# Kernel optimization log

Measured on AMD Instinct MI355X. Metric: run time of the kernel, lower is better.

## Reference

```python
import jax, jax.numpy as jnp
import numpy as np

X_DIM, Y_DIM, HIDDEN, N = 768, 768, 300, 768


def setup_inputs() -> dict:
    key = jax.random.key(0)
    ks = jax.random.split(key, 7)
    lim1 = 1.0 / np.sqrt(X_DIM + Y_DIM)
    lim2 = 1.0 / np.sqrt(HIDDEN)
    return {
        "x_samples": jax.random.normal(ks[0], (N, X_DIM), dtype=jnp.float32),
        "y_samples": jax.random.normal(ks[1], (N, Y_DIM), dtype=jnp.float32),
        "perm": jax.random.permutation(ks[2], N).astype(jnp.int32),
        # Linear 1: (x_dim+y_dim) -> hidden, torch default uniform init
        "W1": jax.random.uniform(ks[3], (HIDDEN, X_DIM + Y_DIM), jnp.float32, -lim1, lim1),
        "b1": jax.random.uniform(ks[4], (HIDDEN,), jnp.float32, -lim1, lim1),
        # Linear 2: hidden -> 1
        "W2": jax.random.uniform(ks[5], (1, HIDDEN), jnp.float32, -lim2, lim2),
        "b2": jax.random.uniform(ks[6], (1,), jnp.float32, -lim2, lim2),
    }


def reference(x_samples, y_samples, perm, W1, b1, W2, b2):
    n = x_samples.shape[0]
    x_dim = x_samples.shape[1]
    # First linear is separable across the concat: split W1 into x- and y-parts.
    hx = x_samples @ W1[:, :x_dim].T            # [N, H]
    hy = y_samples @ W1[:, x_dim:].T            # [N, H]
    w2 = W2[0]                                   # [H]
    # T0: matched pairs (x_i, y_i)
    t0 = jax.nn.softplus(jax.nn.relu(hx + hy + b1) @ w2 + b2[0])   # [N]
    # T1[i, j] = F(x_j, y_perm[i]) -- pairwise tile, [N, N, H] intermediate
    hyp = hy[perm]                               # [N, H]
    hpair = jax.nn.relu(hyp[:, None, :] + hx[None, :, :] + b1)     # [N, N, H]
    t1 = jax.nn.softplus(hpair @ w2 + b2[0])     # [N, N]
    lower_bound = t0.mean() - (jax.nn.logsumexp(t1, axis=1).mean() - jnp.log(n).astype(t1.dtype))
    return lower_bound
```

## Files before the change

kernel.cpp:

```cpp
#include <hip/hip_runtime.h>
#include <math.h>

#define NN   768
#define HH   300
#define HP   320
#define KD   768

#define P_OFF    0
#define PKS_STR  245760
#define PG_STR   983040
#define CF_OFF   1966080
#define AF_OFF   2211840
#define RS_OFF   2457600
#define T0_OFF   2469888

__global__ __launch_bounds__(256) void k1_gemm(
    const float* __restrict__ x, const float* __restrict__ y,
    const int* __restrict__ perm, const float* __restrict__ W1,
    float* __restrict__ wsf)
{
    const int tid = threadIdx.x;
    const int tx = tid & 15;
    const int ty = tid >> 4;
    const int i0 = blockIdx.x * 128;
    const int h0 = blockIdx.y * 64;
    const int g  = blockIdx.z & 1;
    const int ks = blockIdx.z >> 1;
    const int kbeg = ks * 192;

    const float* src = g ? y : x;
    const int koff = g ? KD : 0;

    __shared__ float Xt[32][132];
    __shared__ float Wt[32][68];

    float acc[4][8];
    #pragma unroll
    for (int r = 0; r < 4; ++r)
        #pragma unroll
        for (int cc = 0; cc < 8; ++cc) acc[r][cc] = 0.f;

    const int kq = (tid & 7) << 2;
    const float* xp[4];
    int xr[4];
    #pragma unroll
    for (int it = 0; it < 4; ++it) {
        int row = ((tid + it*256) >> 3);
        int gr = i0 + row;
        if (g) gr = perm[gr];
        xp[it] = src + (size_t)gr * KD + kbeg + kq;
        xr[it] = row;
    }
    const float* wp[2];
    int wr[2]; bool wv[2];
    #pragma unroll
    for (int it = 0; it < 2; ++it) {
        int hrow = ((tid + it*256) >> 3);
        int hg = h0 + hrow;
        wv[it] = hg < HH;
        wp[it] = W1 + (size_t)(wv[it] ? hg : 0) * (2*KD) + koff + kbeg + kq;
        wr[it] = hrow;
    }

    for (int kb = 0; kb < 192; kb += 32) {
        float4 xv[4], wvv[2];
        #pragma unroll
        for (int it = 0; it < 4; ++it) xv[it] = *(const float4*)(xp[it] + kb);
        #pragma unroll
        for (int it = 0; it < 2; ++it) {
            wvv[it] = *(const float4*)(wp[it] + kb);
            if (!wv[it]) wvv[it] = make_float4(0,0,0,0);
        }
        if (kb) __syncthreads();
        #pragma unroll
        for (int it = 0; it < 4; ++it) {
            Xt[kq+0][xr[it]] = xv[it].x; Xt[kq+1][xr[it]] = xv[it].y;
            Xt[kq+2][xr[it]] = xv[it].z; Xt[kq+3][xr[it]] = xv[it].w;
        }
        #pragma unroll
        for (int it = 0; it < 2; ++it) {
            Wt[kq+0][wr[it]] = wvv[it].x; Wt[kq+1][wr[it]] = wvv[it].y;
            Wt[kq+2][wr[it]] = wvv[it].z; Wt[kq+3][wr[it]] = wvv[it].w;
        }
        __syncthreads();

        #pragma unroll 8
        for (int k = 0; k < 32; ++k) {
            float4 a   = *(const float4*)&Wt[k][4*ty];
            float4 b0  = *(const float4*)&Xt[k][4*tx];
            float4 b1v = *(const float4*)&Xt[k][64 + 4*tx];
            float ar[4] = {a.x, a.y, a.z, a.w};
            float br[8] = {b0.x, b0.y, b0.z, b0.w, b1v.x, b1v.y, b1v.z, b1v.w};
            #pragma unroll
            for (int r = 0; r < 4; ++r)
                #pragma unroll
                for (int cc = 0; cc < 8; ++cc)
                    acc[r][cc] = fmaf(ar[r], br[cc], acc[r][cc]);
        }
    }

    float* dst = wsf + P_OFF + (size_t)(g*4 + ks) * PKS_STR;
    #pragma unroll
    for (int cc = 0; cc < 8; ++cc) {
        int i = i0 + ((cc >> 2) ? 64 : 0) + 4*tx + (cc & 3);
        float4 v = make_float4(acc[0][cc], acc[1][cc], acc[2][cc], acc[3][cc]);
        *(float4*)(dst + (size_t)i * HP + h0 + 4*ty) = v;
    }
}

__global__ __launch_bounds__(256) void k1b_combine(
    const float* __restrict__ b1, float* __restrict__ wsf)
{
    int idx = blockIdx.x * 256 + threadIdx.x;
    int g = idx >= 61440;
    int rem = idx - g * 61440;
    int i = rem / 80;
    int h4 = (rem % 80) * 4;

    float4 o = make_float4(0.f,0.f,0.f,0.f);
    const float* p = wsf + P_OFF + (size_t)g * PG_STR + (size_t)i * HP + h4;
    #pragma unroll
    for (int ks = 0; ks < 4; ++ks) {
        float4 v = *(const float4*)(p + (size_t)ks * PKS_STR);
        o.x += v.x; o.y += v.y; o.z += v.z; o.w += v.w;
    }
    if (g && h4 < HH) {
        float4 bv = *(const float4*)(b1 + h4);
        o.x += bv.x; o.y += bv.y; o.z += bv.z; o.w += bv.w;
    }
    float* dst = wsf + (g ? AF_OFF : CF_OFF) + (size_t)i * HP + h4;
    *(float4*)dst = o;
}

__global__ __launch_bounds__(512, 2) void k2_pair(
    const float* __restrict__ wsf, const float* __restrict__ w2,
    const int* __restrict__ perm, const float* __restrict__ b2,
    float* __restrict__ rsO, float* __restrict__ t0c)
{
    const int tid  = threadIdx.x;
    const int half = tid >> 8;
    const int t2   = tid & 255;
    const int tx = t2 & 15;
    const int ty = t2 >> 4;
    const int j0 = blockIdx.x * 48;
    const int i0 = blockIdx.y * 48;
    const int hbeg = half * 152;

    const float* AF = wsf + AF_OFF;
    const float* CF = wsf + CF_OFF;

    __shared__ __align__(16) float As[2][48][156];
    __shared__ __align__(16) float Cs[2][48][156];
    __shared__ __align__(16) float w2s[304];

    if (tid < 76) {
        float4 wv = make_float4(0.f,0.f,0.f,0.f);
        if (tid < 75) wv = *(const float4*)(w2 + 4*tid);
        *(float4*)&w2s[4*tid] = wv;
    }
    for (int e = t2; e < 48 * 38; e += 256) {
        int i = e / 38, q = e % 38;
        *(float4*)&As[half][i][4*q] =
            *(const float4*)(AF + (size_t)(i0 + i) * HP + hbeg + 4*q);
        *(float4*)&Cs[half][i][4*q] =
            *(const float4*)(CF + (size_t)(j0 + i) * HP + hbeg + 4*q);
    }
    __syncthreads();

    float acc[3][3];
    #pragma unroll
    for (int r = 0; r < 3; ++r)
        #pragma unroll
        for (int c = 0; c < 3; ++c) acc[r][c] = 0.f;

    #pragma unroll 2
    for (int k = 0; k < 38; ++k) {
        float4 wq = *(const float4*)&w2s[hbeg + 4*k];
        float4 a0 = *(const float4*)&As[half][ty     ][4*k];
        float4 a1 = *(const float4*)&As[half][ty + 16][4*k];
        float4 a2 = *(const float4*)&As[half][ty + 32][4*k];
        float4 c0 = *(const float4*)&Cs[half][tx     ][4*k];
        float4 c1 = *(const float4*)&Cs[half][tx + 16][4*k];
        float4 c2 = *(const float4*)&Cs[half][tx + 32][4*k];
        const float* wp  = (const float*)&wq;
        const float* ap0 = (const float*)&a0;
        const float* ap1 = (const float*)&a1;
        const float* ap2 = (const float*)&a2;
        const float* cp0 = (const float*)&c0;
        const float* cp1 = (const float*)&c1;
        const float* cp2 = (const float*)&c2;
        #pragma unroll
        for (int hh = 0; hh < 4; ++hh) {
            float wh = wp[hh];
            float av0 = ap0[hh], av1 = ap1[hh], av2 = ap2[hh];
            float cv0 = cp0[hh], cv1 = cp1[hh], cv2 = cp2[hh];
            acc[0][0] = fmaf(fmaxf(av0 + cv0, 0.f), wh, acc[0][0]);
            acc[0][1] = fmaf(fmaxf(av0 + cv1, 0.f), wh, acc[0][1]);
            acc[0][2] = fmaf(fmaxf(av0 + cv2, 0.f), wh, acc[0][2]);
            acc[1][0] = fmaf(fmaxf(av1 + cv0, 0.f), wh, acc[1][0]);
            acc[1][1] = fmaf(fmaxf(av1 + cv1, 0.f), wh, acc[1][1]);
            acc[1][2] = fmaf(fmaxf(av1 + cv2, 0.f), wh, acc[1][2]);
            acc[2][0] = fmaf(fmaxf(av2 + cv0, 0.f), wh, acc[2][0]);
            acc[2][1] = fmaf(fmaxf(av2 + cv1, 0.f), wh, acc[2][1]);
            acc[2][2] = fmaf(fmaxf(av2 + cv2, 0.f), wh, acc[2][2]);
        }
    }

    __syncthreads();
    float* comb = &As[0][0][0];
    if (half) {
        float* cp = comb + t2 * 9;
        #pragma unroll
        for (int r = 0; r < 3; ++r)
            #pragma unroll
            for (int c = 0; c < 3; ++c) cp[r*3 + c] = acc[r][c];
    }
    __syncthreads();

    if (half == 0) {
        const float* cp = comb + t2 * 9;
        const float b2v = b2[0];
        #pragma unroll
        for (int r = 0; r < 3; ++r) {
            int i = i0 + ty + 16 * r;
            int pj = perm[i];
            float rsum = 0.f;
            #pragma unroll
            for (int c = 0; c < 3; ++c) {
                int j = j0 + tx + 16 * c;
                float u = acc[r][c] + cp[r*3 + c] + b2v;
                rsum += expf(u);
                if (j == pj)
                    t0c[i] = (u > 0.f) ? u + log1pf(expf(-u)) : log1pf(expf(u));
            }
            #pragma unroll
            for (int off = 8; off; off >>= 1)
                rsum += __shfl_xor(rsum, off, 16);
            if (tx == 0) rsO[(size_t)blockIdx.x * NN + i] = rsum;
        }
    }
}

__global__ __launch_bounds__(256) void k3_final(
    const float* __restrict__ wsf, float* __restrict__ out)
{
    const int tid = threadIdx.x;
    const float* rs = wsf + RS_OFF;
    const float* t0 = wsf + T0_OFF;

    double st0 = 0.0, slse = 0.0;
    for (int i = tid; i < NN; i += 256) {
        float s = 0.f;
        #pragma unroll
        for (int jb = 0; jb < 16; ++jb) s += rs[(size_t)jb * NN + i];
        st0  += (double)t0[i];
        slse += log((double)NN + (double)s);
    }
    __shared__ double sa[256], sb[256];
    sa[tid] = st0; sb[tid] = slse;
    __syncthreads();
    for (int s = 128; s > 0; s >>= 1) {
        if (tid < s) { sa[tid] += sa[tid+s]; sb[tid] += sb[tid+s]; }
        __syncthreads();
    }
    if (tid == 0) {
        double lb = sa[0]/(double)NN - (sb[0]/(double)NN - log((double)NN));
        out[0] = (float)lb;
    }
}

extern "C" void kernel_launch(void* const* d_in, const int* in_sizes, int n_in,
                              void* d_out, int out_size, void* d_ws, size_t ws_size,
                              hipStream_t stream) {
    const float* x    = (const float*)d_in[0];
    const float* y    = (const float*)d_in[1];
    const int*   perm = (const int*)  d_in[2];
    const float* W1   = (const float*)d_in[3];
    const float* b1   = (const float*)d_in[4];
    const float* W2   = (const float*)d_in[5];
    const float* b2   = (const float*)d_in[6];
    float* wsf = (float*)d_ws;
    float* out = (float*)d_out;

    k1_gemm    <<<dim3(6,5,8),  256, 0, stream>>>(x, y, perm, W1, wsf);
    k1b_combine<<<480,          256, 0, stream>>>(b1, wsf);
    k2_pair    <<<dim3(16,16),  512, 0, stream>>>(wsf, W2, perm, b2,
                                                  wsf + RS_OFF, wsf + T0_OFF);
    k3_final   <<<1,            256, 0, stream>>>(wsf, out);
}
```

Measured before the change: 115.5 us.

## Transpose pair-kernel LDS tiles to k-major and software-pipeline the inner loop

```diff
diff --git a/kernel.cpp b/kernel.cpp
--- a/kernel.cpp
+++ b/kernel.cpp
@@ -132,7 +132,33 @@
     *(float4*)dst = o;
 }
 
-__global__ __launch_bounds__(512, 2) void k2_pair(
+#define ROW(wv, a0v, a1v, a2v, c0v, c1v, c2v)                      \
+    acc00 = fmaf(fmaxf(a0v + c0v, 0.f), wv, acc00);                \
+    acc01 = fmaf(fmaxf(a0v + c1v, 0.f), wv, acc01);                \
+    acc02 = fmaf(fmaxf(a0v + c2v, 0.f), wv, acc02);                \
+    acc10 = fmaf(fmaxf(a1v + c0v, 0.f), wv, acc10);                \
+    acc11 = fmaf(fmaxf(a1v + c1v, 0.f), wv, acc11);                \
+    acc12 = fmaf(fmaxf(a1v + c2v, 0.f), wv, acc12);                \
+    acc20 = fmaf(fmaxf(a2v + c0v, 0.f), wv, acc20);                \
+    acc21 = fmaf(fmaxf(a2v + c1v, 0.f), wv, acc21);                \
+    acc22 = fmaf(fmaxf(a2v + c2v, 0.f), wv, acc22);
+
+#define COMPQ(W, A0, A1, A2, C0, C1, C2)                           \
+    ROW(W.x, A0.x, A1.x, A2.x, C0.x, C1.x, C2.x)                   \
+    ROW(W.y, A0.y, A1.y, A2.y, C0.y, C1.y, C2.y)                   \
+    ROW(W.z, A0.z, A1.z, A2.z, C0.z, C1.z, C2.z)                   \
+    ROW(W.w, A0.w, A1.w, A2.w, C0.w, C1.w, C2.w)
+
+#define LOADQ(W, A0, A1, A2, C0, C1, C2, q)                        \
+    W  = *(const float4*)&w2s[hbeg + 4*(q)];                       \
+    A0 = *(const float4*)&Aq[half][q][ty][0];                      \
+    A1 = *(const float4*)&Aq[half][q][ty + 16][0];                 \
+    A2 = *(const float4*)&Aq[half][q][ty + 32][0];                 \
+    C0 = *(const float4*)&Cq[half][q][tx][0];                      \
+    C1 = *(const float4*)&Cq[half][q][tx + 16][0];                 \
+    C2 = *(const float4*)&Cq[half][q][tx + 32][0];
+
+__global__ __launch_bounds__(512) void k2_pair(
     const float* __restrict__ wsf, const float* __restrict__ w2,
     const int* __restrict__ perm, const float* __restrict__ b2,
     float* __restrict__ rsO, float* __restrict__ t0c)
@@ -149,8 +175,8 @@
     const float* AF = wsf + AF_OFF;
     const float* CF = wsf + CF_OFF;
 
-    __shared__ __align__(16) float As[2][48][156];
-    __shared__ __align__(16) float Cs[2][48][156];
+    __shared__ __align__(16) float Aq[2][38][49][4];
+    __shared__ __align__(16) float Cq[2][38][49][4];
     __shared__ __align__(16) float w2s[304];
 
     if (tid < 76) {
@@ -160,64 +186,44 @@
     }
     for (int e = t2; e < 48 * 38; e += 256) {
         int i = e / 38, q = e % 38;
-        *(float4*)&As[half][i][4*q] =
-            *(const float4*)(AF + (size_t)(i0 + i) * HP + hbeg + 4*q);
-        *(float4*)&Cs[half][i][4*q] =
-            *(const float4*)(CF + (size_t)(j0 + i) * HP + hbeg + 4*q);
-    }
-    __syncthreads();
-
-    float acc[3][3];
-    #pragma unroll
-    for (int r = 0; r < 3; ++r)
-        #pragma unroll
-        for (int c = 0; c < 3; ++c) acc[r][c] = 0.f;
-
-    #pragma unroll 2
-    for (int k = 0; k < 38; ++k) {
-        float4 wq = *(const float4*)&w2s[hbeg + 4*k];
-        float4 a0 = *(const float4*)&As[half][ty     ][4*k];
-        float4 a1 = *(const float4*)&As[half][ty + 16][4*k];
-        float4 a2 = *(const float4*)&As[half][ty + 32][4*k];
-        float4 c0 = *(const float4*)&Cs[half][tx     ][4*k];
-        float4 c1 = *(const float4*)&Cs[half][tx + 16][4*k];
-        float4 c2 = *(const float4*)&Cs[half][tx + 32][4*k];
-        const float* wp  = (const float*)&wq;
-        const float* ap0 = (const float*)&a0;
-        const float* ap1 = (const float*)&a1;
-        const float* ap2 = (const float*)&a2;
-        const float* cp0 = (const float*)&c0;
-        const float* cp1 = (const float*)&c1;
-        const float* cp2 = (const float*)&c2;
-        #pragma unroll
-        for (int hh = 0; hh < 4; ++hh) {
-            float wh = wp[hh];
-            float av0 = ap0[hh], av1 = ap1[hh], av2 = ap2[hh];
-            float cv0 = cp0[hh], cv1 = cp1[hh], cv2 = cp2[hh];
-            acc[0][0] = fmaf(fmaxf(av0 + cv0, 0.f), wh, acc[0][0]);
-            acc[0][1] = fmaf(fmaxf(av0 + cv1, 0.f), wh, acc[0][1]);
-            acc[0][2] = fmaf(fmaxf(av0 + cv2, 0.f), wh, acc[0][2]);
-            acc[1][0] = fmaf(fmaxf(av1 + cv0, 0.f), wh, acc[1][0]);
-            acc[1][1] = fmaf(fmaxf(av1 + cv1, 0.f), wh, acc[1][1]);
-            acc[1][2] = fmaf(fmaxf(av1 + cv2, 0.f), wh, acc[1][2]);
-            acc[2][0] = fmaf(fmaxf(av2 + cv0, 0.f), wh, acc[2][0]);
-            acc[2][1] = fmaf(fmaxf(av2 + cv1, 0.f), wh, acc[2][1]);
-            acc[2][2] = fmaf(fmaxf(av2 + cv2, 0.f), wh, acc[2][2]);
-        }
-    }
-
-    __syncthreads();
-    float* comb = &As[0][0][0];
+        float4 av = *(const float4*)(AF + (size_t)(i0 + i) * HP + hbeg + 4*q);
+        float4 cv = *(const float4*)(CF + (size_t)(j0 + i) * HP + hbeg + 4*q);
+        *(float4*)&Aq[half][q][i][0] = av;
+        *(float4*)&Cq[half][q][i][0] = cv;
+    }
+    __syncthreads();
+
+    float acc00 = 0.f, acc01 = 0.f, acc02 = 0.f;
+    float acc10 = 0.f, acc11 = 0.f, acc12 = 0.f;
+    float acc20 = 0.f, acc21 = 0.f, acc22 = 0.f;
+
+    float4 w0, a00, a10, a20, c00, c10, c20;
+    float4 w1, a01, a11, a21, c01, c11, c21;
+    LOADQ(w0, a00, a10, a20, c00, c10, c20, 0)
+    for (int q = 0; q < 36; q += 2) {
+        LOADQ(w1, a01, a11, a21, c01, c11, c21, q + 1)
+        COMPQ(w0, a00, a10, a20, c00, c10, c20)
+        LOADQ(w0, a00, a10, a20, c00, c10, c20, q + 2)
+        COMPQ(w1, a01, a11, a21, c01, c11, c21)
+    }
+    LOADQ(w1, a01, a11, a21, c01, c11, c21, 37)
+    COMPQ(w0, a00, a10, a20, c00, c10, c20)
+    COMPQ(w1, a01, a11, a21, c01, c11, c21)
+
+    __syncthreads();
+    float* comb = &Aq[0][0][0][0];
     if (half) {
         float* cp = comb + t2 * 9;
-        #pragma unroll
-        for (int r = 0; r < 3; ++r)
-            #pragma unroll
-            for (int c = 0; c < 3; ++c) cp[r*3 + c] = acc[r][c];
+        cp[0] = acc00; cp[1] = acc01; cp[2] = acc02;
+        cp[3] = acc10; cp[4] = acc11; cp[5] = acc12;
+        cp[6] = acc20; cp[7] = acc21; cp[8] = acc22;
     }
     __syncthreads();
 
     if (half == 0) {
+        const float accA[3][3] = {{acc00, acc01, acc02},
+                                  {acc10, acc11, acc12},
+                                  {acc20, acc21, acc22}};
         const float* cp = comb + t2 * 9;
         const float b2v = b2[0];
         #pragma unroll
@@ -228,7 +234,7 @@
             #pragma unroll
             for (int c = 0; c < 3; ++c) {
                 int j = j0 + tx + 16 * c;
-                float u = acc[r][c] + cp[r*3 + c] + b2v;
+                float u = accA[r][c] + cp[r*3 + c] + b2v;
                 rsum += expf(u);
                 if (j == pj)
                     t0c[i] = (u > 0.f) ? u + log1pf(expf(-u)) : log1pf(expf(u));
```

Result: no change. 116.7 us (+1.0%).

## Fuse split-K combine and final reduction into pair kernel with atomics

Applied to the files above, without the earlier changes.

```diff
diff --git a/kernel.cpp b/kernel.cpp
--- a/kernel.cpp
+++ b/kernel.cpp
@@ -9,10 +9,9 @@
 #define P_OFF    0
 #define PKS_STR  245760
 #define PG_STR   983040
-#define CF_OFF   1966080
-#define AF_OFF   2211840
-#define RS_OFF   2457600
-#define T0_OFF   2469888
+#define ES_OFF   1966080
+#define CT_OFF   1966848
+#define DS_OFF   1966880
 
 __global__ __launch_bounds__(256) void k1_gemm(
     const float* __restrict__ x, const float* __restrict__ y,
@@ -20,6 +19,9 @@
     float* __restrict__ wsf)
 {
     const int tid = threadIdx.x;
+    if (blockIdx.x == 0 && blockIdx.y == 0 && blockIdx.z == 0) {
+        for (int z = tid; z < 864; z += 256) wsf[ES_OFF + z] = 0.f;
+    }
     const int tx = tid & 15;
     const int ty = tid >> 4;
     const int i0 = blockIdx.x * 128;
@@ -108,34 +110,10 @@
     }
 }
 
-__global__ __launch_bounds__(256) void k1b_combine(
-    const float* __restrict__ b1, float* __restrict__ wsf)
-{
-    int idx = blockIdx.x * 256 + threadIdx.x;
-    int g = idx >= 61440;
-    int rem = idx - g * 61440;
-    int i = rem / 80;
-    int h4 = (rem % 80) * 4;
-
-    float4 o = make_float4(0.f,0.f,0.f,0.f);
-    const float* p = wsf + P_OFF + (size_t)g * PG_STR + (size_t)i * HP + h4;
-    #pragma unroll
-    for (int ks = 0; ks < 4; ++ks) {
-        float4 v = *(const float4*)(p + (size_t)ks * PKS_STR);
-        o.x += v.x; o.y += v.y; o.z += v.z; o.w += v.w;
-    }
-    if (g && h4 < HH) {
-        float4 bv = *(const float4*)(b1 + h4);
-        o.x += bv.x; o.y += bv.y; o.z += bv.z; o.w += bv.w;
-    }
-    float* dst = wsf + (g ? AF_OFF : CF_OFF) + (size_t)i * HP + h4;
-    *(float4*)dst = o;
-}
-
-__global__ __launch_bounds__(512, 2) void k2_pair(
-    const float* __restrict__ wsf, const float* __restrict__ w2,
-    const int* __restrict__ perm, const float* __restrict__ b2,
-    float* __restrict__ rsO, float* __restrict__ t0c)
+__global__ __launch_bounds__(512) void k2_pair(
+    float* __restrict__ wsf, const float* __restrict__ w2,
+    const int* __restrict__ perm, const float* __restrict__ b1,
+    const float* __restrict__ b2, float* __restrict__ out)
 {
     const int tid  = threadIdx.x;
     const int half = tid >> 8;
@@ -144,14 +122,18 @@
     const int ty = t2 >> 4;
     const int j0 = blockIdx.x * 48;
     const int i0 = blockIdx.y * 48;
-    const int hbeg = half * 152;
-
-    const float* AF = wsf + AF_OFF;
-    const float* CF = wsf + CF_OFF;
+
+    const float* PC = wsf + P_OFF;
+    const float* PA = wsf + P_OFF + PG_STR;
+    float* esF   = wsf + ES_OFF;
+    int*   ctr   = (int*)(wsf + CT_OFF);
+    double* t0s  = (double*)(wsf + DS_OFF);
+    double* lses = (double*)(wsf + DS_OFF) + 1;
 
     __shared__ __align__(16) float As[2][48][156];
     __shared__ __align__(16) float Cs[2][48][156];
     __shared__ __align__(16) float w2s[304];
+    __shared__ int finflag;
 
     if (tid < 76) {
         float4 wv = make_float4(0.f,0.f,0.f,0.f);
@@ -160,10 +142,27 @@
     }
     for (int e = t2; e < 48 * 38; e += 256) {
         int i = e / 38, q = e % 38;
-        *(float4*)&As[half][i][4*q] =
-            *(const float4*)(AF + (size_t)(i0 + i) * HP + hbeg + 4*q);
-        *(float4*)&Cs[half][i][4*q] =
-            *(const float4*)(CF + (size_t)(j0 + i) * HP + hbeg + 4*q);
+        int Q = half * 38 + q;
+        size_t oa = (size_t)(i0 + i) * HP + 4*Q;
+        float4 a0 = *(const float4*)(PA + oa);
+        float4 a1 = *(const float4*)(PA + PKS_STR + oa);
+        float4 a2 = *(const float4*)(PA + 2*(size_t)PKS_STR + oa);
+        float4 a3 = *(const float4*)(PA + 3*(size_t)PKS_STR + oa);
+        float4 av = make_float4(a0.x+a1.x+a2.x+a3.x, a0.y+a1.y+a2.y+a3.y,
+                                a0.z+a1.z+a2.z+a3.z, a0.w+a1.w+a2.w+a3.w);
+        if (Q < 75) {
+            float4 bq = *(const float4*)(b1 + 4*Q);
+            av.x += bq.x; av.y += bq.y; av.z += bq.z; av.w += bq.w;
+        }
+        size_t oc = (size_t)(j0 + i) * HP + 4*Q;
+        float4 c0 = *(const float4*)(PC + oc);
+        float4 c1 = *(const float4*)(PC + PKS_STR + oc);
+        float4 c2 = *(const float4*)(PC + 2*(size_t)PKS_STR + oc);
+        float4 c3 = *(const float4*)(PC + 3*(size_t)PKS_STR + oc);
+        float4 cv = make_float4(c0.x+c1.x+c2.x+c3.x, c0.y+c1.y+c2.y+c3.y,
+                                c0.z+c1.z+c2.z+c3.z, c0.w+c1.w+c2.w+c3.w);
+        *(float4*)&As[half][i][4*q] = av;
+        *(float4*)&Cs[half][i][4*q] = cv;
     }
     __syncthreads();
 
@@ -173,6 +172,7 @@
         #pragma unroll
         for (int c = 0; c < 3; ++c) acc[r][c] = 0.f;
 
+    const int hbeg = half * 152;
     #pragma unroll 2
     for (int k = 0; k < 38; ++k) {
         float4 wq = *(const float4*)&w2s[hbeg + 4*k];
@@ -230,42 +230,48 @@
                 int j = j0 + tx + 16 * c;
                 float u = acc[r][c] + cp[r*3 + c] + b2v;
                 rsum += expf(u);
-                if (j == pj)
-                    t0c[i] = (u > 0.f) ? u + log1pf(expf(-u)) : log1pf(expf(u));
+                if (j == pj) {
+                    float sp = (u > 0.f) ? u + log1pf(expf(-u)) : log1pf(expf(u));
+                    atomicAdd(t0s, (double)sp);
+                }
             }
             #pragma unroll
             for (int off = 8; off; off >>= 1)
                 rsum += __shfl_xor(rsum, off, 16);
-            if (tx == 0) rsO[(size_t)blockIdx.x * NN + i] = rsum;
-        }
-    }
-}
-
-__global__ __launch_bounds__(256) void k3_final(
-    const float* __restrict__ wsf, float* __restrict__ out)
-{
-    const int tid = threadIdx.x;
-    const float* rs = wsf + RS_OFF;
-    const float* t0 = wsf + T0_OFF;
-
-    double st0 = 0.0, slse = 0.0;
-    for (int i = tid; i < NN; i += 256) {
-        float s = 0.f;
-        #pragma unroll
-        for (int jb = 0; jb < 16; ++jb) s += rs[(size_t)jb * NN + i];
-        st0  += (double)t0[i];
-        slse += log((double)NN + (double)s);
-    }
-    __shared__ double sa[256], sb[256];
-    sa[tid] = st0; sb[tid] = slse;
-    __syncthreads();
-    for (int s = 128; s > 0; s >>= 1) {
-        if (tid < s) { sa[tid] += sa[tid+s]; sb[tid] += sb[tid+s]; }
-        __syncthreads();
-    }
+            if (tx == 0) atomicAdd(&esF[i], rsum);
+        }
+    }
+
+    __syncthreads();
     if (tid == 0) {
-        double lb = sa[0]/(double)NN - (sb[0]/(double)NN - log((double)NN));
-        out[0] = (float)lb;
+        __threadfence();
+        int old = atomicAdd(&ctr[blockIdx.y], 1);
+        finflag = (old == 15);
+    }
+    __syncthreads();
+    if (finflag && tid < 64) {
+        __threadfence();
+        double lp = 0.0;
+        if (tid < 48) {
+            float e = atomicAdd(&esF[i0 + tid], 0.0f);
+            lp = log((double)NN + (double)e);
+        }
+        #pragma unroll
+        for (int off = 32; off; off >>= 1)
+            lp += __shfl_down(lp, off);
+        if (tid == 0) {
+            atomicAdd(lses, lp);
+            __threadfence();
+            int o2 = atomicAdd(&ctr[16], 1);
+            if (o2 == 15) {
+                __threadfence();
+                double t0v = atomicAdd(t0s, 0.0);
+                double lsv = atomicAdd(lses, 0.0);
+                double lb = t0v / (double)NN
+                          - (lsv / (double)NN - log((double)NN));
+                out[0] = (float)lb;
+            }
+        }
     }
 }
 
@@ -282,9 +288,6 @@
     float* wsf = (float*)d_ws;
     float* out = (float*)d_out;
 
-    k1_gemm    <<<dim3(6,5,8),  256, 0, stream>>>(x, y, perm, W1, wsf);
-    k1b_combine<<<480,          256, 0, stream>>>(b1, wsf);
-    k2_pair    <<<dim3(16,16),  512, 0, stream>>>(wsf, W2, perm, b2,
-                                                  wsf + RS_OFF, wsf + T0_OFF);
-    k3_final   <<<1,            256, 0, stream>>>(wsf, out);
+    k1_gemm <<<dim3(6,5,8),  256, 0, stream>>>(x, y, perm, W1, wsf);
+    k2_pair <<<dim3(16,16),  512, 0, stream>>>(wsf, W2, perm, b1, b2, out);
 }
```

Measured after the change: 127.4 us. 10.3% more time.

## Enlarge GEMM tile to 256x64 with 8x8 microtile and 8-way split-K

Applied to the files above, without the earlier changes.

```diff
diff --git a/kernel.cpp b/kernel.cpp
--- a/kernel.cpp
+++ b/kernel.cpp
@@ -8,43 +8,43 @@
 
 #define P_OFF    0
 #define PKS_STR  245760
-#define PG_STR   983040
-#define CF_OFF   1966080
-#define AF_OFF   2211840
-#define RS_OFF   2457600
-#define T0_OFF   2469888
-
-__global__ __launch_bounds__(256) void k1_gemm(
+#define PG_STR   1966080
+#define CF_OFF   3932160
+#define AF_OFF   4177920
+#define RS_OFF   4423680
+#define T0_OFF   4435968
+
+__global__ __launch_bounds__(256, 1) void k1_gemm(
     const float* __restrict__ x, const float* __restrict__ y,
     const int* __restrict__ perm, const float* __restrict__ W1,
     float* __restrict__ wsf)
 {
     const int tid = threadIdx.x;
-    const int tx = tid & 15;
-    const int ty = tid >> 4;
-    const int i0 = blockIdx.x * 128;
+    const int tx = tid & 31;
+    const int ty = tid >> 5;
+    const int i0 = blockIdx.x * 256;
     const int h0 = blockIdx.y * 64;
     const int g  = blockIdx.z & 1;
     const int ks = blockIdx.z >> 1;
-    const int kbeg = ks * 192;
+    const int kbeg = ks * 96;
 
     const float* src = g ? y : x;
     const int koff = g ? KD : 0;
 
-    __shared__ float Xt[32][132];
+    __shared__ float Xt[32][260];
     __shared__ float Wt[32][68];
 
-    float acc[4][8];
-    #pragma unroll
-    for (int r = 0; r < 4; ++r)
-        #pragma unroll
-        for (int cc = 0; cc < 8; ++cc) acc[r][cc] = 0.f;
+    float acc[8][8];
+    #pragma unroll
+    for (int r = 0; r < 8; ++r)
+        #pragma unroll
+        for (int c = 0; c < 8; ++c) acc[r][c] = 0.f;
 
     const int kq = (tid & 7) << 2;
-    const float* xp[4];
-    int xr[4];
-    #pragma unroll
-    for (int it = 0; it < 4; ++it) {
+    const float* xp[8];
+    int xr[8];
+    #pragma unroll
+    for (int it = 0; it < 8; ++it) {
         int row = ((tid + it*256) >> 3);
         int gr = i0 + row;
         if (g) gr = perm[gr];
@@ -62,10 +62,10 @@
         wr[it] = hrow;
     }
 
-    for (int kb = 0; kb < 192; kb += 32) {
-        float4 xv[4], wvv[2];
-        #pragma unroll
-        for (int it = 0; it < 4; ++it) xv[it] = *(const float4*)(xp[it] + kb);
+    for (int kb = 0; kb < 96; kb += 32) {
+        float4 xv[8], wvv[2];
+        #pragma unroll
+        for (int it = 0; it < 8; ++it) xv[it] = *(const float4*)(xp[it] + kb);
         #pragma unroll
         for (int it = 0; it < 2; ++it) {
             wvv[it] = *(const float4*)(wp[it] + kb);
@@ -73,7 +73,7 @@
         }
         if (kb) __syncthreads();
         #pragma unroll
-        for (int it = 0; it < 4; ++it) {
+        for (int it = 0; it < 8; ++it) {
             Xt[kq+0][xr[it]] = xv[it].x; Xt[kq+1][xr[it]] = xv[it].y;
             Xt[kq+2][xr[it]] = xv[it].z; Xt[kq+3][xr[it]] = xv[it].w;
         }
@@ -84,27 +84,33 @@
         }
         __syncthreads();
 
-        #pragma unroll 8
+        #pragma unroll 4
         for (int k = 0; k < 32; ++k) {
-            float4 a   = *(const float4*)&Wt[k][4*ty];
-            float4 b0  = *(const float4*)&Xt[k][4*tx];
-            float4 b1v = *(const float4*)&Xt[k][64 + 4*tx];
-            float ar[4] = {a.x, a.y, a.z, a.w};
-            float br[8] = {b0.x, b0.y, b0.z, b0.w, b1v.x, b1v.y, b1v.z, b1v.w};
-            #pragma unroll
-            for (int r = 0; r < 4; ++r)
+            float4 wlo = *(const float4*)&Wt[k][4*ty];
+            float4 whi = *(const float4*)&Wt[k][32 + 4*ty];
+            float4 xlo = *(const float4*)&Xt[k][4*tx];
+            float4 xhi = *(const float4*)&Xt[k][128 + 4*tx];
+            float hr[8] = {wlo.x, wlo.y, wlo.z, wlo.w,
+                           whi.x, whi.y, whi.z, whi.w};
+            float ir[8] = {xlo.x, xlo.y, xlo.z, xlo.w,
+                           xhi.x, xhi.y, xhi.z, xhi.w};
+            #pragma unroll
+            for (int r = 0; r < 8; ++r)
                 #pragma unroll
-                for (int cc = 0; cc < 8; ++cc)
-                    acc[r][cc] = fmaf(ar[r], br[cc], acc[r][cc]);
-        }
-    }
-
-    float* dst = wsf + P_OFF + (size_t)(g*4 + ks) * PKS_STR;
-    #pragma unroll
-    for (int cc = 0; cc < 8; ++cc) {
-        int i = i0 + ((cc >> 2) ? 64 : 0) + 4*tx + (cc & 3);
-        float4 v = make_float4(acc[0][cc], acc[1][cc], acc[2][cc], acc[3][cc]);
-        *(float4*)(dst + (size_t)i * HP + h0 + 4*ty) = v;
+                for (int c = 0; c < 8; ++c)
+                    acc[r][c] = fmaf(hr[r], ir[c], acc[r][c]);
+        }
+    }
+
+    float* dst = wsf + P_OFF + (size_t)(g*8 + ks) * PKS_STR;
+    #pragma unroll
+    for (int c = 0; c < 8; ++c) {
+        int i = i0 + ((c >> 2) ? 128 : 0) + 4*tx + (c & 3);
+        float* rp = dst + (size_t)i * HP + h0;
+        *(float4*)(rp + 4*ty) =
+            make_float4(acc[0][c], acc[1][c], acc[2][c], acc[3][c]);
+        *(float4*)(rp + 32 + 4*ty) =
+            make_float4(acc[4][c], acc[5][c], acc[6][c], acc[7][c]);
     }
 }
 
@@ -120,7 +126,7 @@
     float4 o = make_float4(0.f,0.f,0.f,0.f);
     const float* p = wsf + P_OFF + (size_t)g * PG_STR + (size_t)i * HP + h4;
     #pragma unroll
-    for (int ks = 0; ks < 4; ++ks) {
+    for (int ks = 0; ks < 8; ++ks) {
         float4 v = *(const float4*)(p + (size_t)ks * PKS_STR);
         o.x += v.x; o.y += v.y; o.z += v.z; o.w += v.w;
     }
@@ -282,7 +288,7 @@
     float* wsf = (float*)d_ws;
     float* out = (float*)d_out;
 
-    k1_gemm    <<<dim3(6,5,8),  256, 0, stream>>>(x, y, perm, W1, wsf);
+    k1_gemm    <<<dim3(3,5,16), 256, 0, stream>>>(x, y, perm, W1, wsf);
     k1b_combine<<<480,          256, 0, stream>>>(b1, wsf);
     k2_pair    <<<dim3(16,16),  512, 0, stream>>>(wsf, W2, perm, b2,
                                                   wsf + RS_OFF, wsf + T0_OFF);
```

Result: faster. 113.0 us (-2.2%).
